# Optimization experiments

Measured on AMD Instinct MI355X. Metric: run time of the kernel, lower is better.

## Reference

```python
import jax, jax.numpy as jnp
from jax import lax
import numpy as np

B, W, F, D = 48, 8192, 64, 128  # batch, input_window, c_in, d_model


def setup_inputs() -> dict:
    key = jax.random.key(0)
    k0, k1, k2, k3 = jax.random.split(key, 4)
    x = jax.random.normal(k0, (B, W, F), jnp.float32)
    # ContextConv(c_in->c_in, k=3): conv1d over time, zero 'same' padding (repo layer, assumed standard conv)
    ctx_w = jax.random.normal(k1, (F, F, 3), jnp.float32) * (2.0 / (F * 3)) ** 0.5
    ctx_b = jnp.zeros((F,), jnp.float32)
    # tokenConv: Conv1d(c_in -> d_model, k=3, circular padding, no bias), kaiming fan_in
    token_w = jax.random.normal(k2, (D, F, 3), jnp.float32) * (2.0 / (F * 3)) ** 0.5
    # seW: Linear(c_in -> input_window)
    seW_w = jax.random.normal(k3, (W, F), jnp.float32) * (1.0 / F) ** 0.5
    seW_b = jnp.zeros((W,), jnp.float32)
    return dict(x=x, ctx_w=ctx_w, ctx_b=ctx_b, token_w=token_w, seW_w=seW_w, seW_b=seW_b)


def _conv1d_ncw(x_ncw, w_oiw, padding):
    return lax.conv_general_dilated(
        x_ncw, w_oiw, window_strides=(1,), padding=padding,
        dimension_numbers=("NCW", "OIW", "NCW"))


def reference(x, ctx_w, ctx_b, token_w, seW_w, seW_b):
    # ---- contextConv: (B,W,F) -> (B,W,F), conv over time ----
    xc = _conv1d_ncw(x.transpose(0, 2, 1), ctx_w, [(1, 1)])  # (B,F,W)
    xc = (xc + ctx_b[None, :, None]).transpose(0, 2, 1)       # (B,W,F)

    # ---- structure_embedding (src is detached in torch) ----
    src = lax.stop_gradient(x)
    srcn = src / jnp.linalg.norm(src, axis=-1, keepdims=True)         # row-normalize each timestep
    gram = jnp.einsum('bwf,bwg->bfg', srcn, srcn)                      # batched f x f matmul
    xse = jax.nn.relu(jnp.einsum('bfg,wg->bfw', gram, seW_w) + seW_b[None, None, :])  # (B,F,W)
    xse = xse.transpose(0, 2, 1)                                       # (B,W,F)

    # ---- tokenConv with circular padding ----
    h = (xc + xse).transpose(0, 2, 1)                                  # (B,F,W)
    hp = jnp.pad(h, ((0, 0), (0, 0), (1, 1)), mode='wrap')
    out = _conv1d_ncw(hp, token_w, 'VALID')                            # (B,D,W)
    return out.transpose(0, 2, 1)                                      # (B,W,D)
```

## Files before the change

### kernel.cpp

```cpp
#include <hip/hip_runtime.h>
#include <stdint.h>

#define Bb 48
#define Ww 8192
#define Ff 64
#define Dd 128
#define TWt 64
#define NSLAB 32

#define WS_GRAMP 0u
#define WS_GRAM  25165824u
#define WS_TWT   25952256u
#define WS_CWT   26001408u
#define WS_GBF   26025984u
#define WS_SWB   26419200u
#define WS_XBF   27467776u
#define WS_TOTAL (27467776ull + 50331648ull)

typedef __bf16 bf16x8 __attribute__((ext_vector_type(8)));
typedef float f32x4 __attribute__((ext_vector_type(4)));

__device__ __forceinline__ float bf2f(unsigned short u){
  union { unsigned int i; float f; } v; v.i = ((unsigned int)u) << 16; return v.f;
}
__device__ __forceinline__ unsigned short f2bf(float f){
  union { float f; unsigned int i; } v; v.f = f;
  unsigned int i = v.i;
  return (unsigned short)((i + 0x7fffu + ((i >> 16) & 1u)) >> 16);
}
__device__ __forceinline__ f32x4 mfma16(bf16x8 a, bf16x8 b, f32x4 c){
  return __builtin_amdgcn_mfma_f32_16x16x32_bf16(a, b, c, 0, 0, 0);
}

__global__ __launch_bounds__(256) void prep_weights(const float* __restrict__ ctx_w,
                                                    const float* __restrict__ token_w,
                                                    const float* __restrict__ seW_w,
                                                    unsigned short* __restrict__ cwT,
                                                    unsigned short* __restrict__ twT,
                                                    unsigned short* __restrict__ sWb,
                                                    int fast)
{
  const int bx = blockIdx.x;
  if (bx < 144){
    int idx = bx * 256 + threadIdx.x;
    const int ntw = Dd * 192;
    if (idx < ntw){
      int d = idx / 192, kim = idx % 192;
      int ktap = kim >> 6, fi = kim & 63;
      twT[idx] = f2bf(token_w[(d * Ff + fi) * 3 + ktap]);
    } else if (idx < ntw + Ff * 192){
      int i2 = idx - ntw;
      int f = i2 / 192, kim = i2 % 192;
      int ktap = kim >> 6, fi = kim & 63;
      cwT[i2] = f2bf(ctx_w[(f * Ff + fi) * 3 + ktap]);
    }
  } else if (fast){
    int i = ((bx - 144) * 256 + threadIdx.x) * 8;
    float4 a0 = *(const float4*)(seW_w + i);
    float4 a1 = *(const float4*)(seW_w + i + 4);
    union { uint4 q; unsigned short s[8]; } u;
    u.s[0]=f2bf(a0.x); u.s[1]=f2bf(a0.y); u.s[2]=f2bf(a0.z); u.s[3]=f2bf(a0.w);
    u.s[4]=f2bf(a1.x); u.s[5]=f2bf(a1.y); u.s[6]=f2bf(a1.z); u.s[7]=f2bf(a1.w);
    *(uint4*)(sWb + i) = u.q;
  }
}

__global__ __launch_bounds__(256) void gram_kernel(const float* __restrict__ x,
                                                   unsigned short* __restrict__ xbf,
                                                   float* __restrict__ gramP,
                                                   int writeXbf)
{
  const int b = blockIdx.y;
  const int w_base = blockIdx.x * (Ww / NSLAB);
  const int t = threadIdx.x;
  const int lane = t & 63;
  const int wave = t >> 6;
  const int lrow = lane & 15;
  const int lk = lane >> 4;

  __shared__ unsigned short st[64 * 72];

  f32x4 acc[4] = {};

  const int wl = t >> 2;
  const int f0 = (t & 3) * 16;

  float v[16];
  {
    const float* xr = x + ((size_t)b * Ww + (size_t)(w_base + wl)) * Ff + f0;
    *(float4*)(v)      = *(const float4*)(xr);
    *(float4*)(v + 4)  = *(const float4*)(xr + 4);
    *(float4*)(v + 8)  = *(const float4*)(xr + 8);
    *(float4*)(v + 12) = *(const float4*)(xr + 12);
  }

  for (int sc = 0; sc < 4; ++sc) {
    const size_t rowg = (size_t)b * Ww + (size_t)(w_base + sc * 64 + wl);

    float ss = 0.f;
#pragma unroll
    for (int i = 0; i < 16; ++i) ss += v[i] * v[i];
    ss += __shfl_xor(ss, 1);
    ss += __shfl_xor(ss, 2);
    float rinv = rsqrtf(ss);

    union { uint4 q[2]; unsigned short s[16]; } u;
#pragma unroll
    for (int i = 0; i < 16; ++i){
      u.s[i] = f2bf(v[i]);
      st[(f0 + i) * 72 + wl] = f2bf(v[i] * rinv);
    }
    if (writeXbf){
      unsigned short* dst = xbf + rowg * Ff + f0;
      *(uint4*)(dst)     = u.q[0];
      *(uint4*)(dst + 8) = u.q[1];
    }

    float vn[16];
    if (sc < 3){
      const float* xr = x + ((size_t)b * Ww + (size_t)(w_base + (sc+1) * 64 + wl)) * Ff + f0;
      *(float4*)(vn)      = *(const float4*)(xr);
      *(float4*)(vn + 4)  = *(const float4*)(xr + 4);
      *(float4*)(vn + 8)  = *(const float4*)(xr + 8);
      *(float4*)(vn + 12) = *(const float4*)(xr + 12);
    }

    __syncthreads();
#pragma unroll
    for (int kc = 0; kc < 2; ++kc){
      const int kw = kc * 32 + lk * 8;
      bf16x8 bfr = *(const bf16x8*)(st + (wave * 16 + lrow) * 72 + kw);
#pragma unroll
      for (int mt = 0; mt < 4; ++mt){
        bf16x8 af = *(const bf16x8*)(st + (mt * 16 + lrow) * 72 + kw);
        acc[mt] = mfma16(af, bfr, acc[mt]);
      }
    }
    __syncthreads();

    if (sc < 3){
#pragma unroll
      for (int i = 0; i < 16; ++i) v[i] = vn[i];
    }
  }

  float* gb = gramP + ((size_t)(blockIdx.x * Bb + b)) * 4096;
#pragma unroll
  for (int mt = 0; mt < 4; ++mt)
#pragma unroll
    for (int r = 0; r < 4; ++r){
      int f = mt * 16 + lk * 4 + r;
      int g = wave * 16 + lrow;
      gb[f * 64 + g] = acc[mt][r];
    }
}

__global__ __launch_bounds__(256) void gram_reduce(const float* __restrict__ gramP,
                                                   float* __restrict__ gram,
                                                   unsigned short* __restrict__ gbf,
                                                   int fast)
{
  int i = blockIdx.x * 256 + threadIdx.x;
  int b = i >> 10;
  int q = i & 1023;
  float sx = 0.f, sy = 0.f, sz = 0.f, sw = 0.f;
#pragma unroll
  for (int sl = 0; sl < NSLAB; ++sl){
    const float4 v = *(const float4*)(gramP + (((size_t)(sl * Bb + b)) << 12) + q * 4);
    sx += v.x; sy += v.y; sz += v.z; sw += v.w;
  }
  float4 s = make_float4(sx, sy, sz, sw);
  *(float4*)(gram + (((size_t)b) << 12) + q * 4) = s;
  if (fast){
    union { unsigned long long u; unsigned short h[4]; } u;
    u.h[0] = f2bf(sx); u.h[1] = f2bf(sy); u.h[2] = f2bf(sz); u.h[3] = f2bf(sw);
    *(unsigned long long*)(gbf + (((size_t)b) << 12) + q * 4) = u.u;
  }
}

#define XSP 72
#define SSP 72
#define HSP 72

__global__ __launch_bounds__(256, 6) void fused_kernel(
    const float* __restrict__ x,
    const unsigned short* __restrict__ xbf,
    const float* __restrict__ ctx_b,
    const float* __restrict__ seW_w,
    const unsigned short* __restrict__ sWb,
    const float* __restrict__ seW_b,
    const float* __restrict__ gram,
    const unsigned short* __restrict__ gbf,
    const unsigned short* __restrict__ cwT,
    const unsigned short* __restrict__ twT,
    float* __restrict__ out,
    int fast)
{
  const int b = blockIdx.y;
  const int w0 = blockIdx.x * TWt;
  const int t = threadIdx.x;
  const int lane = t & 63;
  const int wave = t >> 6;
  const int lrow = lane & 15;
  const int lk = lane >> 4;

  __shared__ __align__(16) unsigned char smem[(84 * XSP + 80 * SSP) * 2];
  unsigned short* xs  = (unsigned short*)smem;
  unsigned short* sws = xs + 84 * XSP;
  unsigned short* hsh = xs;

  if (fast){
    for (int item = t; item < 84 * 8; item += 256){
      int i = item >> 3, seg = item & 7;
      int c = w0 - 2 + i;
      uint4 val = make_uint4(0u,0u,0u,0u);
      if (c >= 0 && c < Ww) val = *(const uint4*)(xbf + ((size_t)b*Ww + c)*Ff + seg*8);
      *(uint4*)(xs + i*XSP + seg*8) = val;
    }
    for (int item = t; item < 80 * 8; item += 256){
      int i = item >> 3, seg = item & 7;
      int hc = (w0 - 1 + i) & (Ww - 1);
      *(uint4*)(sws + i*SSP + seg*8) = *(const uint4*)(sWb + (size_t)hc*Ff + seg*8);
    }
  } else {
    for (int item = t; item < 84 * 8; item += 256){
      int i = item >> 3, seg = item & 7;
      int c = w0 - 2 + i;
      union { uint4 q; unsigned short s[8]; } u;
      if (c >= 0 && c < Ww){
        const float* xr = x + ((size_t)b*Ww + c)*Ff + seg*8;
        float4 a0 = *(const float4*)(xr);
        float4 a1 = *(const float4*)(xr + 4);
        u.s[0]=f2bf(a0.x); u.s[1]=f2bf(a0.y); u.s[2]=f2bf(a0.z); u.s[3]=f2bf(a0.w);
        u.s[4]=f2bf(a1.x); u.s[5]=f2bf(a1.y); u.s[6]=f2bf(a1.z); u.s[7]=f2bf(a1.w);
      } else {
        u.q = make_uint4(0u,0u,0u,0u);
      }
      *(uint4*)(xs + i*XSP + seg*8) = u.q;
    }
  }
  __syncthreads();

  const int nt = wave;
  bf16x8 cw_frag[6];
  {
    const unsigned short* p = cwT + (nt*16 + lrow)*192 + lk*8;
#pragma unroll
    for (int kc = 0; kc < 6; ++kc) cw_frag[kc] = *(const bf16x8*)(p + kc*32);
  }
  bf16x8 se_frag[2];
  if (fast){
    const unsigned short* gp = gbf + (size_t)b*4096 + (nt*16 + lrow)*64;
#pragma unroll
    for (int kc = 0; kc < 2; ++kc) se_frag[kc] = *(const bf16x8*)(gp + kc*32 + lk*8);
  } else {
    const float* gb = gram + (size_t)b * 4096;
#pragma unroll
    for (int kc = 0; kc < 2; ++kc){
      union { bf16x8 v; unsigned short s[8]; } u;
#pragma unroll
      for (int j = 0; j < 8; ++j){
        int g = kc*32 + lk*8 + j;
        u.s[j] = f2bf(gb[g*64 + nt*16 + lrow]);
      }
      se_frag[kc] = u.v;
    }
  }

  f32x4 xc_acc[5] = {};
  f32x4 se_acc[5] = {};

#pragma unroll
  for (int mt = 0; mt < 5; ++mt){
#pragma unroll
    for (int kc = 0; kc < 6; ++kc){
      int kim = kc*32 + lk*8;
      int ktap = kim >> 6, fi = kim & 63;
      bf16x8 a = *(const bf16x8*)(xs + (mt*16 + lrow + ktap)*XSP + fi);
      xc_acc[mt] = mfma16(a, cw_frag[kc], xc_acc[mt]);
    }
    if (fast){
#pragma unroll
      for (int kc = 0; kc < 2; ++kc){
        bf16x8 a = *(const bf16x8*)(sws + (mt*16 + lrow)*SSP + kc*32 + lk*8);
        se_acc[mt] = mfma16(a, se_frag[kc], se_acc[mt]);
      }
    } else {
      int hc = (w0 - 1 + mt*16 + lrow) & (Ww - 1);
      const float* sp = seW_w + (size_t)hc * Ff;
#pragma unroll
      for (int kc = 0; kc < 2; ++kc){
        union { bf16x8 v; unsigned short s[8]; } u;
        float4 a0 = *(const float4*)(sp + kc*32 + lk*8);
        float4 a1 = *(const float4*)(sp + kc*32 + lk*8 + 4);
        u.s[0]=f2bf(a0.x); u.s[1]=f2bf(a0.y); u.s[2]=f2bf(a0.z); u.s[3]=f2bf(a0.w);
        u.s[4]=f2bf(a1.x); u.s[5]=f2bf(a1.y); u.s[6]=f2bf(a1.z); u.s[7]=f2bf(a1.w);
        se_acc[mt] = mfma16(u.v, se_frag[kc], se_acc[mt]);
      }
    }
  }

  __syncthreads();

  {
    float cb = ctx_b[nt*16 + lrow];
#pragma unroll
    for (int mt = 0; mt < 5; ++mt){
#pragma unroll
      for (int r = 0; r < 4; ++r){
        int j = mt*16 + lk*4 + r;
        if (j < 66){
          int hc = (w0 - 1 + j) & (Ww - 1);
          float se = se_acc[mt][r] + seW_b[hc];
          se = se > 0.f ? se : 0.f;
          hsh[j*HSP + nt*16 + lrow] = f2bf(xc_acc[mt][r] + cb + se);
        }
      }
    }
  }
  __syncthreads();

  if (blockIdx.x == 0 || blockIdx.x == (Ww/TWt - 1)){
    const int j  = (blockIdx.x == 0) ? 0 : 65;
    const int hc = (blockIdx.x == 0) ? (Ww - 1) : 0;
    if (t < 64){
      const int f = t;
      float a = ctx_b[f];
      for (int ktap = 0; ktap < 3; ++ktap){
        int c = hc + ktap - 1;
        if (c >= 0 && c < Ww){
          const float* xr = x + ((size_t)b*Ww + c)*Ff;
          const unsigned short* wr = cwT + f*192 + ktap*64;
          for (int fi = 0; fi < 64; ++fi) a += xr[fi] * bf2f(wr[fi]);
        }
      }
      const float* gb = gram + (size_t)b * 4096;
      const float* sp = seW_w + (size_t)hc * Ff;
      float se = seW_b[hc];
      for (int g = 0; g < 64; ++g) se += sp[g] * gb[g*64 + f];
      se = se > 0.f ? se : 0.f;
      hsh[j*HSP + f] = f2bf(a + se);
    }
    __syncthreads();
  }

  bf16x8 tw_frag[2][6];
#pragma unroll
  for (int q = 0; q < 2; ++q){
    const unsigned short* p = twT + ((wave*2 + q)*16 + lrow)*192 + lk*8;
#pragma unroll
    for (int kc = 0; kc < 6; ++kc) tw_frag[q][kc] = *(const bf16x8*)(p + kc*32);
  }
  f32x4 oacc[4][2] = {};
#pragma unroll
  for (int mt = 0; mt < 4; ++mt){
#pragma unroll
    for (int kc = 0; kc < 6; ++kc){
      int kim = kc*32 + lk*8;
      int ktap = kim >> 6, fi = kim & 63;
      bf16x8 a = *(const bf16x8*)(hsh + (mt*16 + lrow + ktap)*HSP + fi);
#pragma unroll
      for (int q = 0; q < 2; ++q)
        oacc[mt][q] = mfma16(a, tw_frag[q][kc], oacc[mt][q]);
    }
  }

#pragma unroll
  for (int mt = 0; mt < 4; ++mt){
#pragma unroll
    for (int q = 0; q < 2; ++q)
#pragma unroll
      for (int r = 0; r < 4; ++r){
        int row = w0 + mt*16 + lk*4 + r;
        int d   = (wave*2 + q)*16 + lrow;
        out[((size_t)b*Ww + row)*Dd + d] = oacc[mt][q][r];
      }
  }
}

extern "C" void kernel_launch(void* const* d_in, const int* in_sizes, int n_in,
                              void* d_out, int out_size, void* d_ws, size_t ws_size,
                              hipStream_t stream)
{
  const float* x       = (const float*)d_in[0];
  const float* ctx_w   = (const float*)d_in[1];
  const float* ctx_b   = (const float*)d_in[2];
  const float* token_w = (const float*)d_in[3];
  const float* seW_w   = (const float*)d_in[4];
  const float* seW_b   = (const float*)d_in[5];
  float* out = (float*)d_out;

  char* ws = (char*)d_ws;
  float*          gramP = (float*)(ws + WS_GRAMP);
  float*          gram  = (float*)(ws + WS_GRAM);
  unsigned short* twT   = (unsigned short*)(ws + WS_TWT);
  unsigned short* cwT   = (unsigned short*)(ws + WS_CWT);
  unsigned short* gbf   = (unsigned short*)(ws + WS_GBF);
  unsigned short* sWb   = (unsigned short*)(ws + WS_SWB);
  unsigned short* xbf   = (unsigned short*)(ws + WS_XBF);

  const int fast = (ws_size >= (size_t)WS_TOTAL) ? 1 : 0;

  prep_weights<<<dim3(400), dim3(256), 0, stream>>>(ctx_w, token_w, seW_w, cwT, twT, sWb, fast);
  gram_kernel<<<dim3(NSLAB, Bb), dim3(256), 0, stream>>>(x, xbf, gramP, fast);
  gram_reduce<<<dim3(192), dim3(256), 0, stream>>>(gramP, gram, gbf, fast);
  fused_kernel<<<dim3(Ww/TWt, Bb), dim3(256), 0, stream>>>(
      x, xbf, ctx_b, seW_w, sWb, seW_b, gram, gbf, cwT, twT, out, fast);
}
```

Before: 382.0 us.

## Use XOR-swizzled LDS layout, give hsh its own buffer, drop a barrier

Replaces the padded 72-element LDS row stride with a 64-wide XOR-swizzled layout in both the gram and fused kernels, aiming to avoid bank conflicts without padding. In the fused kernel, the h tile gets its own LDS region instead of aliasing the x tile, so the barrier before writing h is removed. LDS per block grows and the occupancy hint drops from 6 to 4 blocks per CU, which may reduce latency hiding.

```diff
diff --git a/kernel.cpp b/kernel.cpp
--- a/kernel.cpp
+++ b/kernel.cpp
@@ -30,6 +30,10 @@
 }
 __device__ __forceinline__ f32x4 mfma16(bf16x8 a, bf16x8 b, f32x4 c){
   return __builtin_amdgcn_mfma_f32_16x16x32_bf16(a, b, c, 0, 0, 0);
+}
+
+__device__ __forceinline__ int swz(int row, int col){
+  return row * 64 + ((((col >> 3) ^ (row & 7))) << 3) + (col & 7);
 }
 
 __global__ __launch_bounds__(256) void prep_weights(const float* __restrict__ ctx_w,
@@ -78,7 +82,7 @@
   const int lrow = lane & 15;
   const int lk = lane >> 4;
 
-  __shared__ unsigned short st[64 * 72];
+  __shared__ unsigned short st[64 * 64];
 
   f32x4 acc[4] = {};
 
@@ -108,7 +112,7 @@
 #pragma unroll
     for (int i = 0; i < 16; ++i){
       u.s[i] = f2bf(v[i]);
-      st[(f0 + i) * 72 + wl] = f2bf(v[i] * rinv);
+      st[swz(f0 + i, wl)] = f2bf(v[i] * rinv);
     }
     if (writeXbf){
       unsigned short* dst = xbf + rowg * Ff + f0;
@@ -129,10 +133,10 @@
 #pragma unroll
     for (int kc = 0; kc < 2; ++kc){
       const int kw = kc * 32 + lk * 8;
-      bf16x8 bfr = *(const bf16x8*)(st + (wave * 16 + lrow) * 72 + kw);
+      bf16x8 bfr = *(const bf16x8*)(st + swz(wave * 16 + lrow, kw));
 #pragma unroll
       for (int mt = 0; mt < 4; ++mt){
-        bf16x8 af = *(const bf16x8*)(st + (mt * 16 + lrow) * 72 + kw);
+        bf16x8 af = *(const bf16x8*)(st + swz(mt * 16 + lrow, kw));
         acc[mt] = mfma16(af, bfr, acc[mt]);
       }
     }
@@ -178,11 +182,7 @@
   }
 }
 
-#define XSP 72
-#define SSP 72
-#define HSP 72
-
-__global__ __launch_bounds__(256, 6) void fused_kernel(
+__global__ __launch_bounds__(256, 4) void fused_kernel(
     const float* __restrict__ x,
     const unsigned short* __restrict__ xbf,
     const float* __restrict__ ctx_b,
@@ -204,10 +204,10 @@
   const int lrow = lane & 15;
   const int lk = lane >> 4;
 
-  __shared__ __align__(16) unsigned char smem[(84 * XSP + 80 * SSP) * 2];
+  __shared__ __align__(16) unsigned char smem[(84 + 80 + 66) * 64 * 2];
   unsigned short* xs  = (unsigned short*)smem;
-  unsigned short* sws = xs + 84 * XSP;
-  unsigned short* hsh = xs;
+  unsigned short* sws = xs + 84 * 64;
+  unsigned short* hsh = sws + 80 * 64;
 
   if (fast){
     for (int item = t; item < 84 * 8; item += 256){
@@ -215,12 +215,12 @@
       int c = w0 - 2 + i;
       uint4 val = make_uint4(0u,0u,0u,0u);
       if (c >= 0 && c < Ww) val = *(const uint4*)(xbf + ((size_t)b*Ww + c)*Ff + seg*8);
-      *(uint4*)(xs + i*XSP + seg*8) = val;
+      *(uint4*)(xs + swz(i, seg*8)) = val;
     }
     for (int item = t; item < 80 * 8; item += 256){
       int i = item >> 3, seg = item & 7;
       int hc = (w0 - 1 + i) & (Ww - 1);
-      *(uint4*)(sws + i*SSP + seg*8) = *(const uint4*)(sWb + (size_t)hc*Ff + seg*8);
+      *(uint4*)(sws + swz(i, seg*8)) = *(const uint4*)(sWb + (size_t)hc*Ff + seg*8);
     }
   } else {
     for (int item = t; item < 84 * 8; item += 256){
@@ -236,7 +236,7 @@
       } else {
         u.q = make_uint4(0u,0u,0u,0u);
       }
-      *(uint4*)(xs + i*XSP + seg*8) = u.q;
+      *(uint4*)(xs + swz(i, seg*8)) = u.q;
     }
   }
   __syncthreads();
@@ -276,13 +276,13 @@
     for (int kc = 0; kc < 6; ++kc){
       int kim = kc*32 + lk*8;
       int ktap = kim >> 6, fi = kim & 63;
-      bf16x8 a = *(const bf16x8*)(xs + (mt*16 + lrow + ktap)*XSP + fi);
+      bf16x8 a = *(const bf16x8*)(xs + swz(mt*16 + lrow + ktap, fi));
       xc_acc[mt] = mfma16(a, cw_frag[kc], xc_acc[mt]);
     }
     if (fast){
 #pragma unroll
       for (int kc = 0; kc < 2; ++kc){
-        bf16x8 a = *(const bf16x8*)(sws + (mt*16 + lrow)*SSP + kc*32 + lk*8);
+        bf16x8 a = *(const bf16x8*)(sws + swz(mt*16 + lrow, kc*32 + lk*8));
         se_acc[mt] = mfma16(a, se_frag[kc], se_acc[mt]);
       }
     } else {
@@ -300,8 +300,6 @@
     }
   }
 
-  __syncthreads();
-
   {
     float cb = ctx_b[nt*16 + lrow];
 #pragma unroll
@@ -313,7 +311,7 @@
           int hc = (w0 - 1 + j) & (Ww - 1);
           float se = se_acc[mt][r] + seW_b[hc];
           se = se > 0.f ? se : 0.f;
-          hsh[j*HSP + nt*16 + lrow] = f2bf(xc_acc[mt][r] + cb + se);
+          hsh[swz(j, nt*16 + lrow)] = f2bf(xc_acc[mt][r] + cb + se);
         }
       }
     }
@@ -339,7 +337,7 @@
       float se = seW_b[hc];
       for (int g = 0; g < 64; ++g) se += sp[g] * gb[g*64 + f];
       se = se > 0.f ? se : 0.f;
-      hsh[j*HSP + f] = f2bf(a + se);
+      hsh[swz(j, f)] = f2bf(a + se);
     }
     __syncthreads();
   }
@@ -358,7 +356,7 @@
     for (int kc = 0; kc < 6; ++kc){
       int kim = kc*32 + lk*8;
       int ktap = kim >> 6, fi = kim & 63;
-      bf16x8 a = *(const bf16x8*)(hsh + (mt*16 + lrow + ktap)*HSP + fi);
+      bf16x8 a = *(const bf16x8*)(hsh + swz(mt*16 + lrow + ktap, fi));
 #pragma unroll
       for (int q = 0; q < 2; ++q)
         oacc[mt][q] = mfma16(a, tw_frag[q][kc], oacc[mt][q]);
```

Result: faster. 362.9 us (-5.0%).
